# Kernel tuning notes

Measured on AMD Instinct MI355X. Metric: run time of the kernel, lower is better.

Reference implementation:

```python
import jax, jax.numpy as jnp
import numpy as np

NUM_CAPSULE = 128   # must equal steps (seq_len) for the reshape in the original code
DIM_CAPSULE = 64
ROUTINGS = 3
EPS = 1e-7          # K.epsilon()


def pos_emb(x):
    """Sinusoidal position embedding added to x over its last two dims [..., S, D].
    Matches the Keras code: evens use sin(pos/10000^(2k/D)), odds use cos with the
    same frequency (odds-1 == 2k), interleaved via stack+reshape."""
    S, D = x.shape[-2], x.shape[-1]
    pos = jnp.arange(S, dtype=x.dtype)[:, None]                      # [S,1]
    inv_freq = 1.0 / jnp.power(10000.0, (2.0 * jnp.arange(D // 2, dtype=x.dtype)) / D)
    ang = pos * inv_freq[None, :]                                    # [S, D/2]
    pe = jnp.stack([jnp.sin(ang), jnp.cos(ang)], axis=-1).reshape(S, D)
    return x + pe


def squash(s):
    ss = jnp.sum(s * s, axis=-1, keepdims=True)
    scale = ss / (1.0 + ss) / jnp.sqrt(ss + EPS)
    return scale * s


def setup_inputs() -> dict:
    key = jax.random.key(0)
    k1, k2 = jax.random.split(key)
    B, steps, in_dim = 32, 128, 256
    u_vecs = jax.random.normal(k1, (B, steps, in_dim), dtype=jnp.float32)
    mask = jnp.ones((B, steps), dtype=jnp.float32)
    # glorot_uniform for capsule kernel (1, in_dim, dim_capsule)
    lim = float(np.sqrt(6.0 / (in_dim + DIM_CAPSULE)))
    W = jax.random.uniform(k2, (1, in_dim, DIM_CAPSULE), jnp.float32, -lim, lim)
    return {"u_vecs": u_vecs, "mask": mask, "W": W}


def reference(u_vecs, mask, W):
    B, steps, in_dim = u_vecs.shape
    N, D = NUM_CAPSULE, DIM_CAPSULE  # N == steps by construction
    # share_weights branch: tile W across steps, permute, add PE, flatten to a conv1d
    # kernel of width 1 -> a plain [in_dim, steps*D] projection matrix.
    tmp = jnp.transpose(jnp.broadcast_to(W, (steps, in_dim, D)), (1, 0, 2))  # [in_dim, steps, D]
    kernel = pos_emb(tmp).reshape(in_dim, steps * D)                          # [in_dim, steps*D]
    u_hat = jnp.einsum('bsi,io->bso', u_vecs, kernel)                         # [B, steps, steps*D]
    u_hat = pos_emb(u_hat)
    u_hat = u_hat.reshape(B, steps, N, D).transpose(0, 2, 1, 3)               # [B, N, In, D]
    b = jnp.zeros((B, N, steps), dtype=u_hat.dtype)                           # routing logits
    m = mask[:, None, :]                                                      # [B, 1, In]
    outputs = None
    for i in range(ROUTINGS):
        # softmax over the num_capsule axis (permute->softmax(-1)->permute in Keras)
        c = jax.nn.softmax(b, axis=1) * m                                     # [B, N, In]
        outputs = squash(jnp.einsum('bni,bnid->bnd', c, u_hat))               # [B, N, D]
        if i < ROUTINGS - 1:
            b = jnp.einsum('bnd,bnid->bni', outputs, u_hat)                   # agreement
    return outputs
```

## Files before the change

### kernel.cpp

```cpp
#include <hip/hip_runtime.h>
#include <math.h>

#define NB 32
#define NS 128
#define NI 256
#define NC 128
#define ND 64

#define L4 9.210340371976184f

__global__ __launch_bounds__(256) void k_prep(const float* __restrict__ u,
                                              const float* __restrict__ W,
                                              float* __restrict__ M,
                                              float* __restrict__ U,
                                              float* __restrict__ PE1) {
    int blk = blockIdx.x;
    int t = threadIdx.x;
    if (blk < 256) {
        __shared__ float us[16][NI];
        __shared__ float ws[128 * ND];
        int r0 = blk * 16;

        {
            const float4* u4 = (const float4*)(u + (size_t)r0 * NI);
            float4* us4 = (float4*)us;
            float up = 0.f;
#pragma unroll
            for (int j = 0; j < 4; ++j) {
                int fi = t * 4 + j;
                float4 v = u4[fi];
                us4[fi] = v;
                up += v.x + v.y + v.z + v.w;
            }
#pragma unroll
            for (int o = 1; o <= 8; o <<= 1) up += __shfl_xor(up, o);
            if ((t & 15) == 0) U[r0 + (t >> 4)] = up;
        }

        int lane = t & 63, w = t >> 6;
        int dp = lane & 31;
        int rh = lane >> 5;
        int rA = w * 4 + rh * 2, rB = rA + 1;
        float2 accA = make_float2(0.f, 0.f), accB = make_float2(0.f, 0.f);
        const float4* W4 = (const float4*)W;

        for (int p = 0; p < 2; ++p) {
            __syncthreads();
            {
                float4* ws4 = (float4*)ws;
#pragma unroll
                for (int j = 0; j < 8; ++j) {
                    int fi = t + 256 * j;
                    ws4[fi] = W4[p * 2048 + fi];
                }
            }
            __syncthreads();
            int ibase = p * 128;
#pragma unroll 8
            for (int ii = 0; ii < 128; ++ii) {
                float2 wv = *(const float2*)&ws[ii * ND + dp * 2];
                float ua = us[rA][ibase + ii];
                float ub = us[rB][ibase + ii];
                accA.x = fmaf(ua, wv.x, accA.x);
                accA.y = fmaf(ua, wv.y, accA.y);
                accB.x = fmaf(ub, wv.x, accB.x);
                accB.y = fmaf(ub, wv.y, accB.y);
            }
        }
        float2* M2 = (float2*)M;
        M2[(size_t)(r0 + rA) * 32 + dp] = accA;
        M2[(size_t)(r0 + rB) * 32 + dp] = accB;
    } else {
        int idx = (blk - 256) * 256 + t;
        int n = idx >> 6, d = idx & 63;
        float ang = (float)n * __expf(-L4 * (float)(d >> 1) * (1.f / 32.f));
        float sv, cv;
        __sincosf(ang, &sv, &cv);
        PE1[idx] = (d & 1) ? cv : sv;
    }
}

__global__ __launch_bounds__(256, 4) void kR(const float* __restrict__ M,
                                             const float* __restrict__ U,
                                             const float* __restrict__ PE1,
                                             const float* __restrict__ cg,
                                             const float* __restrict__ mask,
                                             float* __restrict__ og,
                                             float* __restrict__ bl,
                                             int first, int last) {
    int bp = blockIdx.x;
    int n  = bp & 127;
    int b0 = (bp >> 7) * 2;
    int t  = threadIdx.x;

    __shared__ float  cs[NS][2];
    __shared__ float  Us[NS][2];
    __shared__ float4 redw[2][4][16];
    __shared__ float4 outs4[2][16];
    __shared__ float  tpar[2][2];
    __shared__ float  sc2[2][2];
    __shared__ float  red2[2][NS * 17];

    {
        int bh = t >> 7, s = t & 127;
        int b = b0 + bh;
        float uu = U[b * NS + s];
        float cv = first ? mask[b * NS + s] * (1.f / 128.f)
                         : cg[(b * NC + n) * NS + s];
        cs[s][bh] = cv;
        Us[s][bh] = uu;
        float p = cv * uu;
#pragma unroll
        for (int o = 32; o > 0; o >>= 1) p += __shfl_xor(p, o);
        if ((t & 63) == 0) tpar[bh][(t >> 6) & 1] = p;
    }

    float4 p14;
    if (t < 32) p14 = ((const float4*)PE1)[n * 16 + (t & 15)];

    int dq = t & 15, sq = t >> 4;
    int s0 = sq * 8;
    int k2 = n * 32 + dq * 2;
    float g0 = __expf(-L4 * (float)k2 * (1.f / 4096.f));
    float g1 = __expf(-L4 * (float)(k2 + 1) * (1.f / 4096.f));
    float sa = __sinf((float)s0 * g0), ca = __cosf((float)s0 * g0);
    float sb = __sinf((float)s0 * g1), cb = __cosf((float)s0 * g1);
    float sg0 = __sinf(g0), cg0 = __cosf(g0);
    float sg1 = __sinf(g1), cg1 = __cosf(g1);
    __syncthreads();

    float4 cc4[4];
    {
        const float4* csp = (const float4*)&cs[s0][0];
        cc4[0] = csp[0]; cc4[1] = csp[1]; cc4[2] = csp[2]; cc4[3] = csp[3];
    }

    const float4* M4a = (const float4*)(M + (size_t)(b0 * NS) * ND) + dq;
    const float4* M4b = M4a + NS * 16;
    float4 va[8], vb[8];
    float4 acc0 = make_float4(0.f, 0.f, 0.f, 0.f);
    float4 acc1 = make_float4(0.f, 0.f, 0.f, 0.f);
#pragma unroll
    for (int i = 0; i < 8; ++i) {
        int s = s0 + i;
        float4 m0 = M4a[s * 16];
        float4 m1 = M4b[s * 16];
        float2 cc = ((const float2*)cc4)[i];
        float4 u0, u1;
        u0.x = m0.x + sa; u0.y = m0.y + ca; u0.z = m0.z + sb; u0.w = m0.w + cb;
        u1.x = m1.x + sa; u1.y = m1.y + ca; u1.z = m1.z + sb; u1.w = m1.w + cb;
        va[i] = u0; vb[i] = u1;
        acc0.x = fmaf(cc.x, u0.x, acc0.x);
        acc0.y = fmaf(cc.x, u0.y, acc0.y);
        acc0.z = fmaf(cc.x, u0.z, acc0.z);
        acc0.w = fmaf(cc.x, u0.w, acc0.w);
        acc1.x = fmaf(cc.y, u1.x, acc1.x);
        acc1.y = fmaf(cc.y, u1.y, acc1.y);
        acc1.z = fmaf(cc.y, u1.z, acc1.z);
        acc1.w = fmaf(cc.y, u1.w, acc1.w);
        float nsa = fmaf(sa, cg0, ca * sg0);
        float nca = fmaf(ca, cg0, -sa * sg0);
        sa = nsa; ca = nca;
        float nsb = fmaf(sb, cg1, cb * sg1);
        float ncb = fmaf(cb, cg1, -sb * sg1);
        sb = nsb; cb = ncb;
    }
#pragma unroll
    for (int o = 16; o <= 32; o <<= 1) {
        acc0.x += __shfl_xor(acc0.x, o); acc0.y += __shfl_xor(acc0.y, o);
        acc0.z += __shfl_xor(acc0.z, o); acc0.w += __shfl_xor(acc0.w, o);
        acc1.x += __shfl_xor(acc1.x, o); acc1.y += __shfl_xor(acc1.y, o);
        acc1.z += __shfl_xor(acc1.z, o); acc1.w += __shfl_xor(acc1.w, o);
    }
    if ((t & 48) == 0) {
        int w = t >> 6;
        redw[0][w][dq] = acc0;
        redw[1][w][dq] = acc1;
    }
    __syncthreads();

    if (t < 32) {
        int bh = t >> 4, q = t & 15;
        float4 r0 = redw[bh][0][q], r1 = redw[bh][1][q];
        float4 r2 = redw[bh][2][q], r3 = redw[bh][3][q];
        float4 o;
        o.x = r0.x + r1.x + r2.x + r3.x;
        o.y = r0.y + r1.y + r2.y + r3.y;
        o.z = r0.z + r1.z + r2.z + r3.z;
        o.w = r0.w + r1.w + r2.w + r3.w;
        float T2 = tpar[bh][0] + tpar[bh][1];
        o.x = fmaf(p14.x, T2, o.x);
        o.y = fmaf(p14.y, T2, o.y);
        o.z = fmaf(p14.z, T2, o.z);
        o.w = fmaf(p14.w, T2, o.w);
        outs4[bh][q] = o;
        float ssq = o.x * o.x + o.y * o.y + o.z * o.z + o.w * o.w;
        float ppu = o.x * p14.x + o.y * p14.y + o.z * p14.z + o.w * p14.w;
#pragma unroll
        for (int o2 = 1; o2 <= 8; o2 <<= 1) {
            ssq += __shfl_xor(ssq, o2);
            ppu += __shfl_xor(ppu, o2);
        }
        if (q == 0) {
            sc2[bh][0] = ssq / (1.f + ssq) * rsqrtf(ssq + 1e-7f);
            sc2[bh][1] = ppu;
        }
    }
    __syncthreads();

    if (last) {
        if (t < 32) {
            int bh = t >> 4, q = t & 15;
            float sc = sc2[bh][0];
            float4 o = outs4[bh][q];
            o.x *= sc; o.y *= sc; o.z *= sc; o.w *= sc;
            ((float4*)og)[((b0 + bh) * NC + n) * 16 + q] = o;
        }
        return;
    }

    float4 oa = outs4[0][dq], ob = outs4[1][dq];
#pragma unroll
    for (int i = 0; i < 8; ++i) {
        int s = s0 + i;
        float4 v0 = va[i], v1 = vb[i];
        red2[0][s * 17 + dq] = v0.x * oa.x + v0.y * oa.y + v0.z * oa.z + v0.w * oa.w;
        red2[1][s * 17 + dq] = v1.x * ob.x + v1.y * ob.y + v1.z * ob.z + v1.w * ob.w;
    }
    __syncthreads();
    {
        int bh = t >> 7, s = t & 127;
        const float* r = &red2[bh][s * 17];
        float sum = 0.f;
#pragma unroll
        for (int q = 0; q < 16; ++q) sum += r[q];
        bl[((b0 + bh) * NC + n) * NS + s] =
            sc2[bh][0] * (sum + sc2[bh][1] * Us[s][bh]);
    }
}

__global__ __launch_bounds__(256) void kS(const float* __restrict__ bl,
                                          const float* __restrict__ mask,
                                          float* __restrict__ c) {
    int blk = blockIdx.x;
    int b = blk >> 3, s0 = (blk & 7) * 16;
    int t = threadIdx.x;

    __shared__ float tl[NC][17];
    __shared__ float pr[16][17];
    __shared__ float ps[16][17];
    __shared__ float itot[16], msk[16];

    if (t < 16) msk[t] = mask[b * NS + s0 + t];
#pragma unroll
    for (int i = 0; i < 8; ++i) {
        int idx = i * 256 + t;
        int n = idx >> 4, si = idx & 15;
        tl[n][si] = bl[(b * NC + n) * NS + s0 + si];
    }
    __syncthreads();

    int si = t & 15, ch = t >> 4;
    float mx = -1e30f;
#pragma unroll
    for (int j = 0; j < 8; ++j) mx = fmaxf(mx, tl[ch * 8 + j][si]);
    pr[ch][si] = mx;
    __syncthreads();

    mx = pr[0][si];
#pragma unroll
    for (int jc = 1; jc < 16; ++jc) mx = fmaxf(mx, pr[jc][si]);
    float sm = 0.f;
#pragma unroll
    for (int j = 0; j < 8; ++j) {
        float e = __expf(tl[ch * 8 + j][si] - mx);
        tl[ch * 8 + j][si] = e;
        sm += e;
    }
    ps[ch][si] = sm;
    __syncthreads();

    if (t < 16) {
        float tot = 0.f;
#pragma unroll
        for (int jc = 0; jc < 16; ++jc) tot += ps[jc][t];
        itot[t] = msk[t] / tot;
    }
    __syncthreads();

#pragma unroll
    for (int i = 0; i < 8; ++i) {
        int idx = i * 256 + t;
        int n = idx >> 4, sj = idx & 15;
        c[(b * NC + n) * NS + s0 + sj] = tl[n][sj] * itot[sj];
    }
}

extern "C" void kernel_launch(void* const* d_in, const int* in_sizes, int n_in,
                              void* d_out, int out_size, void* d_ws, size_t ws_size,
                              hipStream_t stream) {
    const float* u    = (const float*)d_in[0];
    const float* mask = (const float*)d_in[1];
    const float* W    = (const float*)d_in[2];
    float* out = (float*)d_out;

    float* ws  = (float*)d_ws;
    float* M   = ws;
    float* U   = M + NB * NS * ND;
    float* PE1 = U + NB * NS;
    float* c   = PE1 + NC * ND;
    float* bl  = c + NB * NC * NS;

    k_prep<<<288, 256, 0, stream>>>(u, W, M, U, PE1);

    kR<<<2048, 256, 0, stream>>>(M, U, PE1, c, mask, out, bl, 1, 0);
    kS<<<NB * 8, 256, 0, stream>>>(bl, mask, c);
    kR<<<2048, 256, 0, stream>>>(M, U, PE1, c, mask, out, bl, 0, 0);
    kS<<<NB * 8, 256, 0, stream>>>(bl, mask, c);
    kR<<<2048, 256, 0, stream>>>(M, U, PE1, c, mask, out, bl, 0, 1);
}
```

Baseline: 99.61 us.

## Replace softmax kernel with per-column stats and fuse normalization into routing kernel

```diff
diff --git a/kernel.cpp b/kernel.cpp
--- a/kernel.cpp
+++ b/kernel.cpp
@@ -80,10 +80,52 @@
     }
 }
 
+__global__ __launch_bounds__(256) void kRed(const float* __restrict__ bl,
+                                            const float* __restrict__ mask,
+                                            float* __restrict__ mx,
+                                            float* __restrict__ minv) {
+    int blk = blockIdx.x;
+    int b = blk >> 2, s0 = (blk & 3) * 32;
+    int t = threadIdx.x;
+    int si = t & 31, nh = t >> 5;
+
+    __shared__ float mxp[8][33];
+    __shared__ float totp[8][33];
+
+    float v[16];
+    float m = -1e30f;
+    const float* base = bl + (size_t)(b * NC + nh * 16) * NS + s0 + si;
+#pragma unroll
+    for (int j = 0; j < 16; ++j) {
+        v[j] = base[j * NS];
+        m = fmaxf(m, v[j]);
+    }
+    mxp[nh][si] = m;
+    __syncthreads();
+
+    float gm = mxp[0][si];
+#pragma unroll
+    for (int k = 1; k < 8; ++k) gm = fmaxf(gm, mxp[k][si]);
+    float sm = 0.f;
+#pragma unroll
+    for (int j = 0; j < 16; ++j) sm += __expf(v[j] - gm);
+    totp[nh][si] = sm;
+    __syncthreads();
+
+    if (t < 32) {
+        float tot = 0.f;
+#pragma unroll
+        for (int k = 0; k < 8; ++k) tot += totp[k][t];
+        mx[b * NS + s0 + t] = gm;
+        minv[b * NS + s0 + t] = mask[b * NS + s0 + t] / tot;
+    }
+}
+
 __global__ __launch_bounds__(256, 4) void kR(const float* __restrict__ M,
                                              const float* __restrict__ U,
                                              const float* __restrict__ PE1,
-                                             const float* __restrict__ cg,
+                                             const float* __restrict__ mxg,
+                                             const float* __restrict__ minvg,
                                              const float* __restrict__ mask,
                                              float* __restrict__ og,
                                              float* __restrict__ bl,
@@ -105,8 +147,13 @@
         int bh = t >> 7, s = t & 127;
         int b = b0 + bh;
         float uu = U[b * NS + s];
-        float cv = first ? mask[b * NS + s] * (1.f / 128.f)
-                         : cg[(b * NC + n) * NS + s];
+        float cv;
+        if (first) {
+            cv = mask[b * NS + s] * (1.f / 128.f);
+        } else {
+            cv = __expf(bl[(size_t)(b * NC + n) * NS + s] - mxg[b * NS + s])
+                 * minvg[b * NS + s];
+        }
         cs[s][bh] = cv;
         Us[s][bh] = uu;
         float p = cv * uu;
@@ -239,63 +286,6 @@
     }
 }
 
-__global__ __launch_bounds__(256) void kS(const float* __restrict__ bl,
-                                          const float* __restrict__ mask,
-                                          float* __restrict__ c) {
-    int blk = blockIdx.x;
-    int b = blk >> 3, s0 = (blk & 7) * 16;
-    int t = threadIdx.x;
-
-    __shared__ float tl[NC][17];
-    __shared__ float pr[16][17];
-    __shared__ float ps[16][17];
-    __shared__ float itot[16], msk[16];
-
-    if (t < 16) msk[t] = mask[b * NS + s0 + t];
-#pragma unroll
-    for (int i = 0; i < 8; ++i) {
-        int idx = i * 256 + t;
-        int n = idx >> 4, si = idx & 15;
-        tl[n][si] = bl[(b * NC + n) * NS + s0 + si];
-    }
-    __syncthreads();
-
-    int si = t & 15, ch = t >> 4;
-    float mx = -1e30f;
-#pragma unroll
-    for (int j = 0; j < 8; ++j) mx = fmaxf(mx, tl[ch * 8 + j][si]);
-    pr[ch][si] = mx;
-    __syncthreads();
-
-    mx = pr[0][si];
-#pragma unroll
-    for (int jc = 1; jc < 16; ++jc) mx = fmaxf(mx, pr[jc][si]);
-    float sm = 0.f;
-#pragma unroll
-    for (int j = 0; j < 8; ++j) {
-        float e = __expf(tl[ch * 8 + j][si] - mx);
-        tl[ch * 8 + j][si] = e;
-        sm += e;
-    }
-    ps[ch][si] = sm;
-    __syncthreads();
-
-    if (t < 16) {
-        float tot = 0.f;
-#pragma unroll
-        for (int jc = 0; jc < 16; ++jc) tot += ps[jc][t];
-        itot[t] = msk[t] / tot;
-    }
-    __syncthreads();
-
-#pragma unroll
-    for (int i = 0; i < 8; ++i) {
-        int idx = i * 256 + t;
-        int n = idx >> 4, sj = idx & 15;
-        c[(b * NC + n) * NS + s0 + sj] = tl[n][sj] * itot[sj];
-    }
-}
-
 extern "C" void kernel_launch(void* const* d_in, const int* in_sizes, int n_in,
                               void* d_out, int out_size, void* d_ws, size_t ws_size,
                               hipStream_t stream) {
@@ -304,18 +294,19 @@
     const float* W    = (const float*)d_in[2];
     float* out = (float*)d_out;
 
-    float* ws  = (float*)d_ws;
-    float* M   = ws;
-    float* U   = M + NB * NS * ND;
-    float* PE1 = U + NB * NS;
-    float* c   = PE1 + NC * ND;
-    float* bl  = c + NB * NC * NS;
+    float* ws   = (float*)d_ws;
+    float* M    = ws;
+    float* U    = M + NB * NS * ND;
+    float* PE1  = U + NB * NS;
+    float* bl   = PE1 + NC * ND;
+    float* mx   = bl + NB * NC * NS;
+    float* minv = mx + NB * NS;
 
     k_prep<<<288, 256, 0, stream>>>(u, W, M, U, PE1);
 
-    kR<<<2048, 256, 0, stream>>>(M, U, PE1, c, mask, out, bl, 1, 0);
-    kS<<<NB * 8, 256, 0, stream>>>(bl, mask, c);
-    kR<<<2048, 256, 0, stream>>>(M, U, PE1, c, mask, out, bl, 0, 0);
-    kS<<<NB * 8, 256, 0, stream>>>(bl, mask, c);
-    kR<<<2048, 256, 0, stream>>>(M, U, PE1, c, mask, out, bl, 0, 1);
+    kR<<<2048, 256, 0, stream>>>(M, U, PE1, mx, minv, mask, out, bl, 1, 0);
+    kRed<<<128, 256, 0, stream>>>(bl, mask, mx, minv);
+    kR<<<2048, 256, 0, stream>>>(M, U, PE1, mx, minv, mask, out, bl, 0, 0);
+    kRed<<<128, 256, 0, stream>>>(bl, mask, mx, minv);
+    kR<<<2048, 256, 0, stream>>>(M, U, PE1, mx, minv, mask, out, bl, 0, 1);
 }
```

After: 98.58 us, median of 2. No clear change (-1.0%).
